# Performance work log

Hardware: AMD Instinct MI355X
Metric: run time of the kernel (lower is better)

Reference implementation:

```python
import jax, jax.numpy as jnp
import numpy as np

EPS = 1e-3  # Keras BatchNormalization default epsilon
K = 7

def _bn(x, gamma, beta, mean, var):
    return gamma * (x - mean) * jax.lax.rsqrt(var + EPS) + beta

def setup_inputs() -> dict:
    key = jax.random.key(0)
    ks = jax.random.split(key, 4)
    B, L, Cin, F = 64, 512, 64, 128
    out_len = L - K + 1
    return {
        "x": jax.random.normal(ks[0], (B, L, Cin), jnp.float32),
        "conv_w": jax.random.normal(ks[1], (K, Cin, F), jnp.float32) * (1.0 / np.sqrt(K * Cin)),
        "conv_b": jnp.zeros((F,), jnp.float32),
        "bn1_gamma": jnp.ones((F,), jnp.float32),
        "bn1_beta": jnp.zeros((F,), jnp.float32),
        "bn1_mean": jnp.zeros((F,), jnp.float32),
        "bn1_var": jnp.ones((F,), jnp.float32),
        "local_w": jax.random.normal(ks[2], (out_len, K * F, F), jnp.float32) * (1.0 / np.sqrt(K * F)),
        "local_b": jnp.zeros((out_len, F), jnp.float32),
        "bn2_gamma": jnp.ones((F,), jnp.float32),
        "bn2_beta": jnp.zeros((F,), jnp.float32),
        "bn2_mean": jnp.zeros((F,), jnp.float32),
        "bn2_var": jnp.ones((F,), jnp.float32),
    }

def reference(x, conv_w, conv_b, bn1_gamma, bn1_beta, bn1_mean, bn1_var,
              local_w, local_b, bn2_gamma, bn2_beta, bn2_mean, bn2_var):
    # Conv1D, padding='same'  (NWC / WIO)
    y = jax.lax.conv_general_dilated(
        x, conv_w, window_strides=(1,), padding="SAME",
        dimension_numbers=("NWC", "WIO", "NWC")) + conv_b
    y = jax.nn.relu(_bn(y, bn1_gamma, bn1_beta, bn1_mean, bn1_var))

    # LocallyConnected1D, padding='valid': per-position unshared weights
    B, L, F = y.shape
    out_len = L - K + 1
    idx = jnp.arange(out_len)[:, None] + jnp.arange(K)[None, :]  # (out_len, K)
    patches = y[:, idx, :].reshape(B, out_len, K * F)             # (B, out_len, K*F)
    z = jnp.einsum("blk,lkf->blf", patches, local_w) + local_b    # (B, out_len, F)
    z = jax.nn.relu(_bn(z, bn2_gamma, bn2_beta, bn2_mean, bn2_var))
    return z
```

## Files before the change

kernel.cpp:

```cpp
#include <hip/hip_runtime.h>
#include <hip/hip_bf16.h>

typedef __attribute__((ext_vector_type(8))) short bf16x8;
typedef __attribute__((ext_vector_type(4))) float f32x4;

#define BB   64
#define LL   512
#define CIN  64
#define FF   128
#define KW   7
#define OUTL 506
#define LPAD 518
#define KC   448
#define KL   896
#define BK   32
#define NCH  28
#define EPSV 1e-3f

#define NPAD  (BB * LPAD * CIN)
#define PADB  (NPAD / 256)
#define NWT   (FF * KC)
#define WTB   (NWT / 256)

static __device__ __forceinline__ short f2bf(float f) {
    unsigned u = __builtin_bit_cast(unsigned, f);
    unsigned r = (u + 0x7fffu + ((u >> 16) & 1u)) >> 16;
    return (short)r;
}

static __device__ __forceinline__ void g2lds16(const float* g, float* l) {
    __builtin_amdgcn_global_load_lds(
        (const __attribute__((address_space(1))) unsigned int*)g,
        (__attribute__((address_space(3))) unsigned int*)l, 16, 0, 0);
}

__global__ void prep_kernel(const float* __restrict__ x, const float* __restrict__ w,
                            short* __restrict__ xp, short* __restrict__ wt) {
    if (blockIdx.x < PADB) {
        int i = blockIdx.x * 256 + threadIdx.x;
        int c  = i & (CIN - 1);
        int t  = i >> 6;
        int lp = t % LPAD;
        int b  = t / LPAD;
        float v = 0.0f;
        int l = lp - 3;
        if (l >= 0 && l < LL) v = x[(b * LL + l) * CIN + c];
        xp[i] = f2bf(v);
    } else {
        int i = (blockIdx.x - PADB) * 256 + threadIdx.x;
        int n = i / KC;
        int k = i - n * KC;
        wt[i] = f2bf(w[(size_t)k * FF + n]);
    }
}

__global__ __launch_bounds__(256) void conv_bn_kernel(
    const short* __restrict__ xp, const short* __restrict__ wt,
    const float* __restrict__ cb, const float* __restrict__ g,
    const float* __restrict__ be, const float* __restrict__ mu,
    const float* __restrict__ va, short* __restrict__ y) {
    const int lane = threadIdx.x & 63;
    const int wid  = threadIdx.x >> 6;
    const int m0   = blockIdx.x * 64;
    const int nb   = wid * 32;
    const int q    = lane >> 4;
    const int ln   = lane & 15;

    const short* arow[4];
#pragma unroll
    for (int mt = 0; mt < 4; ++mt) {
        int m = m0 + mt * 16 + ln;
        int b = m >> 9, l = m & 511;
        arow[mt] = xp + (b * LPAD + l) * CIN;
    }
    const short* brow[2];
#pragma unroll
    for (int nt = 0; nt < 2; ++nt)
        brow[nt] = wt + (size_t)(nb + nt * 16 + ln) * KC;

    f32x4 acc[4][2];
#pragma unroll
    for (int mt = 0; mt < 4; ++mt)
#pragma unroll
        for (int nt = 0; nt < 2; ++nt) acc[mt][nt] = (f32x4){0.f, 0.f, 0.f, 0.f};

#pragma unroll 2
    for (int kc = 0; kc < KC; kc += 32) {
        const int ko = kc + q * 8;
        bf16x8 a[4], bf[2];
#pragma unroll
        for (int mt = 0; mt < 4; ++mt) a[mt] = *(const bf16x8*)(arow[mt] + ko);
#pragma unroll
        for (int nt = 0; nt < 2; ++nt) bf[nt] = *(const bf16x8*)(brow[nt] + ko);
#pragma unroll
        for (int mt = 0; mt < 4; ++mt)
#pragma unroll
            for (int nt = 0; nt < 2; ++nt)
                acc[mt][nt] = __builtin_amdgcn_mfma_f32_16x16x32_bf16(
                    a[mt], bf[nt], acc[mt][nt], 0, 0, 0);
    }

#pragma unroll
    for (int nt = 0; nt < 2; ++nt) {
        const int n = nb + nt * 16 + ln;
        const float s  = g[n] * rsqrtf(va[n] + EPSV);
        const float b2 = s * (cb[n] - mu[n]) + be[n];
#pragma unroll
        for (int mt = 0; mt < 4; ++mt) {
            const int mbase = m0 + mt * 16 + q * 4;
#pragma unroll
            for (int r = 0; r < 4; ++r) {
                float v = fmaxf(acc[mt][nt][r] * s + b2, 0.0f);
                y[(size_t)(mbase + r) * FF + n] = f2bf(v);
            }
        }
    }
}

__global__ __launch_bounds__(256) void local_bn_kernel(
    const short* __restrict__ y, const float* __restrict__ lw,
    const float* __restrict__ lb, const float* __restrict__ g,
    const float* __restrict__ be, const float* __restrict__ mu,
    const float* __restrict__ va, float* __restrict__ out) {
    __shared__ float wtile[2][BK * FF];
    const int l    = blockIdx.x;
    const int lane = threadIdx.x & 63;
    const int wid  = threadIdx.x >> 6;
    const int nb   = wid * 32;
    const int q    = lane >> 4;
    const int ln   = lane & 15;

    const float* wl = lw + (size_t)l * (KL * FF);

    const short* arow[4];
#pragma unroll
    for (int mt = 0; mt < 4; ++mt)
        arow[mt] = y + (size_t)(mt * 16 + ln) * (LL * FF) + (size_t)l * FF;

    f32x4 acc[4][2];
#pragma unroll
    for (int mt = 0; mt < 4; ++mt)
#pragma unroll
        for (int nt = 0; nt < 2; ++nt) acc[mt][nt] = (f32x4){0.f, 0.f, 0.f, 0.f};

    {
        const float* src = wl;
#pragma unroll
        for (int r = 0; r < 4; ++r)
            g2lds16(src + (size_t)(r * 256 + wid * 64 + lane) * 4,
                    &wtile[0][(r * 256 + wid * 64) * 4]);
    }

    for (int c = 0; c < NCH; ++c) {
        __syncthreads();
        if (c + 1 < NCH) {
            const float* src = wl + (size_t)(c + 1) * (BK * FF);
            float* dst = wtile[(c + 1) & 1];
#pragma unroll
            for (int r = 0; r < 4; ++r)
                g2lds16(src + (size_t)(r * 256 + wid * 64 + lane) * 4,
                        &dst[(r * 256 + wid * 64) * 4]);
        }
        const float* wb = wtile[c & 1];
        const int ko = c * BK + q * 8;

        bf16x8 a[4];
#pragma unroll
        for (int mt = 0; mt < 4; ++mt) a[mt] = *(const bf16x8*)(arow[mt] + ko);

        bf16x8 bf[2];
#pragma unroll
        for (int nt = 0; nt < 2; ++nt) {
            const int n = nb + nt * 16 + ln;
#pragma unroll
            for (int j = 0; j < 8; ++j)
                bf[nt][j] = f2bf(wb[(q * 8 + j) * FF + n]);
        }
#pragma unroll
        for (int mt = 0; mt < 4; ++mt)
#pragma unroll
            for (int nt = 0; nt < 2; ++nt)
                acc[mt][nt] = __builtin_amdgcn_mfma_f32_16x16x32_bf16(
                    a[mt], bf[nt], acc[mt][nt], 0, 0, 0);
    }

#pragma unroll
    for (int nt = 0; nt < 2; ++nt) {
        const int n = nb + nt * 16 + ln;
        const float s  = g[n] * rsqrtf(va[n] + EPSV);
        const float b2 = s * (lb[(size_t)l * FF + n] - mu[n]) + be[n];
#pragma unroll
        for (int mt = 0; mt < 4; ++mt) {
            const int bbase = mt * 16 + q * 4;
#pragma unroll
            for (int r = 0; r < 4; ++r) {
                float v = fmaxf(acc[mt][nt][r] * s + b2, 0.0f);
                out[(size_t)(bbase + r) * (OUTL * FF) + (size_t)l * FF + n] = v;
            }
        }
    }
}

extern "C" void kernel_launch(void* const* d_in, const int* in_sizes, int n_in,
                              void* d_out, int out_size, void* d_ws, size_t ws_size,
                              hipStream_t stream) {
    const float* x       = (const float*)d_in[0];
    const float* conv_w  = (const float*)d_in[1];
    const float* conv_b  = (const float*)d_in[2];
    const float* bn1_g   = (const float*)d_in[3];
    const float* bn1_b   = (const float*)d_in[4];
    const float* bn1_m   = (const float*)d_in[5];
    const float* bn1_v   = (const float*)d_in[6];
    const float* local_w = (const float*)d_in[7];
    const float* local_b = (const float*)d_in[8];
    const float* bn2_g   = (const float*)d_in[9];
    const float* bn2_b   = (const float*)d_in[10];
    const float* bn2_m   = (const float*)d_in[11];
    const float* bn2_v   = (const float*)d_in[12];
    float* out = (float*)d_out;

    short* xp  = (short*)d_ws;
    short* ybf = xp + (size_t)NPAD;
    short* wt  = ybf + (size_t)BB * LL * FF;

    prep_kernel<<<PADB + WTB, 256, 0, stream>>>(x, conv_w, xp, wt);
    conv_bn_kernel<<<(BB * LL) / 64, 256, 0, stream>>>(
        xp, wt, conv_b, bn1_g, bn1_b, bn1_m, bn1_v, ybf);
    local_bn_kernel<<<OUTL, 256, 0, stream>>>(
        ybf, local_w, local_b, bn2_g, bn2_b, bn2_m, bn2_v, out);
}
```

Baseline: 374.8 us.

## Split locally-connected kernel across two N-halves per position with deeper K tiles

The locally-connected GEMM now launches two blocks per output position, each computing 64 of the 128 filters, so twice as many blocks share the memory-bound weight stream across the GPU's compute units. Each block stages 64x64 fp32 weight tiles (14 chunks) instead of 32x128 (28 chunks), halving the barrier count per block. Activation rows are loaded by both halves, doubling those reads, and each wave keeps one accumulator column instead of two.

Result: no change. 381.4 us (+1.8%).

```diff
diff --git a/kernel.cpp b/kernel.cpp
--- a/kernel.cpp
+++ b/kernel.cpp
@@ -13,8 +13,8 @@
 #define LPAD 518
 #define KC   448
 #define KL   896
-#define BK   32
-#define NCH  28
+#define BK2  64
+#define NCH2 14
 #define EPSV 1e-3f
 
 #define NPAD  (BB * LPAD * CIN)
@@ -122,83 +122,75 @@
     const float* __restrict__ lb, const float* __restrict__ g,
     const float* __restrict__ be, const float* __restrict__ mu,
     const float* __restrict__ va, float* __restrict__ out) {
-    __shared__ float wtile[2][BK * FF];
-    const int l    = blockIdx.x;
+    __shared__ float wtile[2][BK2 * 64];
+    const int bx   = blockIdx.x;
+    const int l    = bx >> 1;
+    const int nh   = bx & 1;
     const int lane = threadIdx.x & 63;
     const int wid  = threadIdx.x >> 6;
-    const int nb   = wid * 32;
     const int q    = lane >> 4;
     const int ln   = lane & 15;
-
-    const float* wl = lw + (size_t)l * (KL * FF);
+    const int nloc = wid * 16 + ln;
+
+    const float* wl = lw + (size_t)l * (KL * FF) + nh * 64;
 
     const short* arow[4];
 #pragma unroll
     for (int mt = 0; mt < 4; ++mt)
         arow[mt] = y + (size_t)(mt * 16 + ln) * (LL * FF) + (size_t)l * FF;
 
-    f32x4 acc[4][2];
-#pragma unroll
-    for (int mt = 0; mt < 4; ++mt)
-#pragma unroll
-        for (int nt = 0; nt < 2; ++nt) acc[mt][nt] = (f32x4){0.f, 0.f, 0.f, 0.f};
-
-    {
-        const float* src = wl;
-#pragma unroll
-        for (int r = 0; r < 4; ++r)
-            g2lds16(src + (size_t)(r * 256 + wid * 64 + lane) * 4,
-                    &wtile[0][(r * 256 + wid * 64) * 4]);
-    }
-
-    for (int c = 0; c < NCH; ++c) {
+    f32x4 acc[4];
+#pragma unroll
+    for (int mt = 0; mt < 4; ++mt) acc[mt] = (f32x4){0.f, 0.f, 0.f, 0.f};
+
+#define STAGE(c, buf)                                                          \
+    {                                                                          \
+        _Pragma("unroll")                                                      \
+        for (int i = 0; i < 4; ++i) {                                          \
+            const float* src =                                                 \
+                wl + (size_t)((c) * BK2 + wid * 16 + i * 4 + q) * FF + ln * 4; \
+            g2lds16(src, &wtile[buf][wid * 1024 + i * 256]);                   \
+        }                                                                      \
+    }
+
+    STAGE(0, 0)
+
+    for (int c = 0; c < NCH2; ++c) {
         __syncthreads();
-        if (c + 1 < NCH) {
-            const float* src = wl + (size_t)(c + 1) * (BK * FF);
-            float* dst = wtile[(c + 1) & 1];
-#pragma unroll
-            for (int r = 0; r < 4; ++r)
-                g2lds16(src + (size_t)(r * 256 + wid * 64 + lane) * 4,
-                        &dst[(r * 256 + wid * 64) * 4]);
+        if (c + 1 < NCH2) STAGE(c + 1, (c + 1) & 1)
+        const float* wb = wtile[c & 1];
+
+#pragma unroll
+        for (int s = 0; s < 2; ++s) {
+            const int ko = c * BK2 + s * 32 + q * 8;
+            bf16x8 a[4];
+#pragma unroll
+            for (int mt = 0; mt < 4; ++mt)
+                a[mt] = *(const bf16x8*)(arow[mt] + ko);
+            bf16x8 bf;
+#pragma unroll
+            for (int j = 0; j < 8; ++j)
+                bf[j] = f2bf(wb[(s * 32 + q * 8 + j) * 64 + nloc]);
+#pragma unroll
+            for (int mt = 0; mt < 4; ++mt)
+                acc[mt] = __builtin_amdgcn_mfma_f32_16x16x32_bf16(
+                    a[mt], bf, acc[mt], 0, 0, 0);
         }
-        const float* wb = wtile[c & 1];
-        const int ko = c * BK + q * 8;
-
-        bf16x8 a[4];
-#pragma unroll
-        for (int mt = 0; mt < 4; ++mt) a[mt] = *(const bf16x8*)(arow[mt] + ko);
-
-        bf16x8 bf[2];
-#pragma unroll
-        for (int nt = 0; nt < 2; ++nt) {
-            const int n = nb + nt * 16 + ln;
-#pragma unroll
-            for (int j = 0; j < 8; ++j)
-                bf[nt][j] = f2bf(wb[(q * 8 + j) * FF + n]);
+    }
+
+    const int n = nh * 64 + nloc;
+    const float sc = g[n] * rsqrtf(va[n] + EPSV);
+    const float b2 = sc * (lb[(size_t)l * FF + n] - mu[n]) + be[n];
+#pragma unroll
+    for (int mt = 0; mt < 4; ++mt) {
+        const int bbase = mt * 16 + q * 4;
+#pragma unroll
+        for (int r = 0; r < 4; ++r) {
+            float v = fmaxf(acc[mt][r] * sc + b2, 0.0f);
+            out[(size_t)(bbase + r) * (OUTL * FF) + (size_t)l * FF + n] = v;
         }
-#pragma unroll
-        for (int mt = 0; mt < 4; ++mt)
-#pragma unroll
-            for (int nt = 0; nt < 2; ++nt)
-                acc[mt][nt] = __builtin_amdgcn_mfma_f32_16x16x32_bf16(
-                    a[mt], bf[nt], acc[mt][nt], 0, 0, 0);
-    }
-
-#pragma unroll
-    for (int nt = 0; nt < 2; ++nt) {
-        const int n = nb + nt * 16 + ln;
-        const float s  = g[n] * rsqrtf(va[n] + EPSV);
-        const float b2 = s * (lb[(size_t)l * FF + n] - mu[n]) + be[n];
-#pragma unroll
-        for (int mt = 0; mt < 4; ++mt) {
-            const int bbase = mt * 16 + q * 4;
-#pragma unroll
-            for (int r = 0; r < 4; ++r) {
-                float v = fmaxf(acc[mt][nt][r] * s + b2, 0.0f);
-                out[(size_t)(bbase + r) * (OUTL * FF) + (size_t)l * FF + n] = v;
-            }
-        }
-    }
+    }
+#undef STAGE
 }
 
 extern "C" void kernel_launch(void* const* d_in, const int* in_sizes, int n_in,
@@ -226,6 +218,6 @@
     prep_kernel<<<PADB + WTB, 256, 0, stream>>>(x, conv_w, xp, wt);
     conv_bn_kernel<<<(BB * LL) / 64, 256, 0, stream>>>(
         xp, wt, conv_b, bn1_g, bn1_b, bn1_m, bn1_v, ybf);
-    local_bn_kernel<<<OUTL, 256, 0, stream>>>(
+    local_bn_kernel<<<OUTL * 2, 256, 0, stream>>>(
         ybf, local_w, local_b, bn2_g, bn2_b, bn2_m, bn2_v, out);
 }
```
